# Kernel tuning notes

Hardware: AMD Instinct MI355X
Metric: run time of the kernel (lower is better)

The kernel has to match this reference:

```python
import jax, jax.numpy as jnp
import numpy as np

B, N, D = 8, 1024, 1024
E, H = 16, 4096
CAP_FACTOR = 1.25  # training-mode capacity factor
NUM_CLASSES = 345


def setup_inputs() -> dict:
    key = jax.random.key(0)
    k1, k2, k3, k4 = jax.random.split(key, 4)
    inputs = jax.random.normal(k1, (B, N, D), dtype=jnp.float32)
    current_y = jax.random.randint(k2, (B,), 0, NUM_CLASSES, dtype=jnp.int32)
    std1 = 1.0 / np.sqrt(H)  # init_ uses 1/sqrt(last dim)
    std2 = 1.0 / np.sqrt(D)
    w1 = jax.random.uniform(k3, (E, D, H), dtype=jnp.float32, minval=-std1, maxval=std1)
    w2 = jax.random.uniform(k4, (E, H, D), dtype=jnp.float32, minval=-std2, maxval=std2)
    return {"inputs": inputs, "current_y": current_y, "w1": w1, "w2": w2}


def reference(inputs, current_y, w1, w2):
    b, n, d = inputs.shape
    e = w1.shape[0]
    cap = max(min(n, int(n * CAP_FACTOR / e)), 4)  # MIN_EXPERT_CAPACITY=4
    dt = inputs.dtype

    # class-based gating: every token of sample i goes to expert y_i % e
    idx = jnp.broadcast_to(jnp.remainder(current_y, e)[:, None], (b, n))  # (b,n)
    oh = jax.nn.one_hot(idx, e, dtype=dt)                                 # (b,n,e)
    # exclusive cumsum over token dim, masked
    pos = (jnp.cumsum(oh, axis=-2) - oh) * oh                             # (b,n,e)
    mask1 = oh * (pos < cap).astype(dt)                                   # drop overflow tokens
    mask1_flat = mask1.sum(axis=-1)                                       # (b,n)
    pos_flat = pos.sum(axis=-1).astype(jnp.int32)                         # (b,n)

    # combine[b,n,e,c]; out-of-range positions -> zero row (safe_one_hot semantics)
    combine = (mask1_flat[..., None, None]
               * oh[..., None]
               * jax.nn.one_hot(pos_flat, cap, dtype=dt)[..., None, :])
    dispatch = (combine > 0).astype(dt)

    # dispatch tokens to padded expert slots: (e, b, cap, d)
    expert_in = jnp.einsum('bnd,bnec->ebcd', inputs, dispatch).reshape(e, b * cap, d)
    hidden = jax.nn.gelu(jnp.einsum('end,edh->enh', expert_in, w1), approximate=False)
    expert_out = jnp.einsum('enh,ehd->end', hidden, w2).reshape(e, b, cap, d)

    output = jnp.einsum('ebcd,bnec->bnd', expert_out, combine)
    return output
```

## Files before the change

kernel.cpp:

```cpp
#include <hip/hip_runtime.h>
#include <hip/hip_bf16.h>

#define NB   8
#define NTOK 1024
#define DDIM 1024
#define NEXP 16
#define HDIM 4096
#define CAP  80
#define BK   64

using bf16x8 = __attribute__((ext_vector_type(8))) __bf16;
using bf16x4 = __attribute__((ext_vector_type(4))) __bf16;
using f32x4  = __attribute__((ext_vector_type(4))) float;

__global__ __launch_bounds__(256) void moe_g1(
    const float* __restrict__ X, const int* __restrict__ Y,
    const float* __restrict__ W1, __bf16* __restrict__ Hid)
{
    const int b     = blockIdx.y;
    const int e     = Y[b] & (NEXP - 1);
    const int nbase = blockIdx.x * 64;
    const int tid   = threadIdx.x;
    const int w     = tid >> 6;
    const int l     = tid & 63;
    const int q     = l >> 4;
    const int r     = l & 15;
    const int n     = nbase + w * 16 + r;

    __shared__ __bf16 As[CAP][BK + 8];

    const float* Xb  = X  + (size_t)b * NTOK * DDIM;
    const float* W1e = W1 + (size_t)e * DDIM * HDIM;

    f32x4 acc[5];
    #pragma unroll
    for (int i = 0; i < 5; ++i) acc[i] = f32x4{0.f, 0.f, 0.f, 0.f};

    for (int k0 = 0; k0 < DDIM; k0 += BK) {
        float bv[16];
        const float* bp = W1e + (size_t)(k0 + q * 8) * HDIM + n;
        #pragma unroll
        for (int s = 0; s < 2; ++s)
            #pragma unroll
            for (int j = 0; j < 8; ++j)
                bv[s * 8 + j] = bp[(size_t)(s * 32 + j) * HDIM];

        __syncthreads();
        #pragma unroll
        for (int it = 0; it < 5; ++it) {
            int i   = tid + 256 * it;
            int row = i >> 4, kg = i & 15;
            float4 v = *(const float4*)&Xb[(size_t)row * DDIM + k0 + kg * 4];
            bf16x4 p = {(__bf16)v.x, (__bf16)v.y, (__bf16)v.z, (__bf16)v.w};
            *(bf16x4*)&As[row][kg * 4] = p;
        }
        __syncthreads();

        #pragma unroll
        for (int s = 0; s < 2; ++s) {
            bf16x8 bf;
            #pragma unroll
            for (int j = 0; j < 8; ++j) bf[j] = (__bf16)bv[s * 8 + j];
            #pragma unroll
            for (int mt = 0; mt < 5; ++mt) {
                bf16x8 af = *(const bf16x8*)&As[mt * 16 + r][s * 32 + q * 8];
                acc[mt] = __builtin_amdgcn_mfma_f32_16x16x32_bf16(af, bf, acc[mt], 0, 0, 0);
            }
        }
    }

    __bf16* Hb = Hid + (size_t)b * CAP * HDIM;
    #pragma unroll
    for (int mt = 0; mt < 5; ++mt)
        #pragma unroll
        for (int v = 0; v < 4; ++v) {
            int m = mt * 16 + q * 4 + v;
            float x = acc[mt][v];
            float g = 0.5f * x * (1.0f + erff(x * 0.70710678118654752f));
            Hb[(size_t)m * HDIM + n] = (__bf16)g;
        }
}

__global__ __launch_bounds__(256) void moe_g2(
    const __bf16* __restrict__ Hid, const int* __restrict__ Y,
    const float* __restrict__ W2, float* __restrict__ Out)
{
    const int b     = blockIdx.y;
    const int e     = Y[b] & (NEXP - 1);
    const int nbase = blockIdx.x * 64;
    const int kz    = blockIdx.z * (HDIM / 4);
    const int tid   = threadIdx.x;
    const int w     = tid >> 6;
    const int l     = tid & 63;
    const int q     = l >> 4;
    const int r     = l & 15;
    const int n     = nbase + w * 16 + r;

    __shared__ __bf16 As[CAP][BK + 8];

    const __bf16* Hb  = Hid + (size_t)b * CAP * HDIM;
    const float*  W2e = W2  + (size_t)e * HDIM * DDIM;

    f32x4 acc[5];
    #pragma unroll
    for (int i = 0; i < 5; ++i) acc[i] = f32x4{0.f, 0.f, 0.f, 0.f};

    for (int k0 = kz; k0 < kz + HDIM / 4; k0 += BK) {
        float bv[16];
        const float* bp = W2e + (size_t)(k0 + q * 8) * DDIM + n;
        #pragma unroll
        for (int s = 0; s < 2; ++s)
            #pragma unroll
            for (int j = 0; j < 8; ++j)
                bv[s * 8 + j] = bp[(size_t)(s * 32 + j) * DDIM];

        __syncthreads();
        #pragma unroll
        for (int it = 0; it < 5; ++it) {
            int i   = tid + 256 * it;
            int row = i >> 4, kg = i & 15;
            uint2 v = *(const uint2*)&Hb[(size_t)row * HDIM + k0 + kg * 4];
            *(uint2*)&As[row][kg * 4] = v;
        }
        __syncthreads();

        #pragma unroll
        for (int s = 0; s < 2; ++s) {
            bf16x8 bf;
            #pragma unroll
            for (int j = 0; j < 8; ++j) bf[j] = (__bf16)bv[s * 8 + j];
            #pragma unroll
            for (int mt = 0; mt < 5; ++mt) {
                bf16x8 af = *(const bf16x8*)&As[mt * 16 + r][s * 32 + q * 8];
                acc[mt] = __builtin_amdgcn_mfma_f32_16x16x32_bf16(af, bf, acc[mt], 0, 0, 0);
            }
        }
    }

    float* Ob = Out + (size_t)b * NTOK * DDIM;
    #pragma unroll
    for (int mt = 0; mt < 5; ++mt)
        #pragma unroll
        for (int v = 0; v < 4; ++v) {
            int m = mt * 16 + q * 4 + v;
            atomicAdd(&Ob[(size_t)m * DDIM + n], acc[mt][v]);
        }
}

extern "C" void kernel_launch(void* const* d_in, const int* in_sizes, int n_in,
                              void* d_out, int out_size, void* d_ws, size_t ws_size,
                              hipStream_t stream) {
    const float* X  = (const float*)d_in[0];
    const int*   Y  = (const int*)d_in[1];
    const float* W1 = (const float*)d_in[2];
    const float* W2 = (const float*)d_in[3];
    float*  Out = (float*)d_out;
    __bf16* Hid = (__bf16*)d_ws;

    hipMemsetAsync(d_out, 0, (size_t)out_size * sizeof(float), stream);

    moe_g1<<<dim3(HDIM / 64, NB), 256, 0, stream>>>(X, Y, W1, Hid);
    moe_g2<<<dim3(DDIM / 64, NB, 4), 256, 0, stream>>>(Hid, Y, W2, Out);
}
```

Measured before the change: 475.2 us.

## Double-buffer LDS tiles with register prefetch and transpose weights via LDS

Both GEMM kernels now stage the weight tile through shared memory. Each thread loads it as float4 vectors and transposes it into a bf16 Bt buffer, replacing the per-thread strided scalar loads. Shared A and B tiles are double-buffered, and the next K-slice is prefetched into registers while MFMAs run on the current buffer, which leaves one barrier per iteration. This aims to improve global load coalescing and overlap memory latency with compute, at the cost of more LDS and registers.

```diff
diff --git a/kernel.cpp b/kernel.cpp
--- a/kernel.cpp
+++ b/kernel.cpp
@@ -8,6 +8,7 @@
 #define HDIM 4096
 #define CAP  80
 #define BK   64
+#define LDA  (BK + 8)
 
 using bf16x8 = __attribute__((ext_vector_type(8))) __bf16;
 using bf16x4 = __attribute__((ext_vector_type(4))) __bf16;
@@ -26,8 +27,13 @@
     const int q     = l >> 4;
     const int r     = l & 15;
     const int n     = nbase + w * 16 + r;
-
-    __shared__ __bf16 As[CAP][BK + 8];
+    const int kb    = tid & 15;
+    const int hb    = tid >> 4;
+    const int arow  = tid >> 4;
+    const int akg   = tid & 15;
+
+    __shared__ __bf16 As[2][CAP][LDA];
+    __shared__ __bf16 Bt[2][64][LDA];
 
     const float* Xb  = X  + (size_t)b * NTOK * DDIM;
     const float* W1e = W1 + (size_t)e * DDIM * HDIM;
@@ -36,37 +42,56 @@
     #pragma unroll
     for (int i = 0; i < 5; ++i) acc[i] = f32x4{0.f, 0.f, 0.f, 0.f};
 
-    for (int k0 = 0; k0 < DDIM; k0 += BK) {
-        float bv[16];
-        const float* bp = W1e + (size_t)(k0 + q * 8) * HDIM + n;
-        #pragma unroll
-        for (int s = 0; s < 2; ++s)
-            #pragma unroll
-            for (int j = 0; j < 8; ++j)
-                bv[s * 8 + j] = bp[(size_t)(s * 32 + j) * HDIM];
-
+    float4 a_reg[5];
+    float4 b_reg[4];
+
+    #pragma unroll
+    for (int it = 0; it < 5; ++it)
+        a_reg[it] = *(const float4*)&Xb[(size_t)(arow + 16 * it) * DDIM + akg * 4];
+    #pragma unroll
+    for (int kk = 0; kk < 4; ++kk)
+        b_reg[kk] = *(const float4*)&W1e[(size_t)(kb * 4 + kk) * HDIM + nbase + hb * 4];
+
+    int cur = 0;
+    for (int t = 0; t < DDIM / BK; ++t) {
+        #pragma unroll
+        for (int it = 0; it < 5; ++it) {
+            float4 v = a_reg[it];
+            bf16x4 p = {(__bf16)v.x, (__bf16)v.y, (__bf16)v.z, (__bf16)v.w};
+            *(bf16x4*)&As[cur][arow + 16 * it][akg * 4] = p;
+        }
+        {
+            bf16x4 p0 = {(__bf16)b_reg[0].x, (__bf16)b_reg[1].x, (__bf16)b_reg[2].x, (__bf16)b_reg[3].x};
+            bf16x4 p1 = {(__bf16)b_reg[0].y, (__bf16)b_reg[1].y, (__bf16)b_reg[2].y, (__bf16)b_reg[3].y};
+            bf16x4 p2 = {(__bf16)b_reg[0].z, (__bf16)b_reg[1].z, (__bf16)b_reg[2].z, (__bf16)b_reg[3].z};
+            bf16x4 p3 = {(__bf16)b_reg[0].w, (__bf16)b_reg[1].w, (__bf16)b_reg[2].w, (__bf16)b_reg[3].w};
+            *(bf16x4*)&Bt[cur][hb * 4 + 0][kb * 4] = p0;
+            *(bf16x4*)&Bt[cur][hb * 4 + 1][kb * 4] = p1;
+            *(bf16x4*)&Bt[cur][hb * 4 + 2][kb * 4] = p2;
+            *(bf16x4*)&Bt[cur][hb * 4 + 3][kb * 4] = p3;
+        }
         __syncthreads();
-        #pragma unroll
-        for (int it = 0; it < 5; ++it) {
-            int i   = tid + 256 * it;
-            int row = i >> 4, kg = i & 15;
-            float4 v = *(const float4*)&Xb[(size_t)row * DDIM + k0 + kg * 4];
-            bf16x4 p = {(__bf16)v.x, (__bf16)v.y, (__bf16)v.z, (__bf16)v.w};
-            *(bf16x4*)&As[row][kg * 4] = p;
-        }
-        __syncthreads();
+
+        if (t + 1 < DDIM / BK) {
+            const int k0 = (t + 1) * BK;
+            #pragma unroll
+            for (int it = 0; it < 5; ++it)
+                a_reg[it] = *(const float4*)&Xb[(size_t)(arow + 16 * it) * DDIM + k0 + akg * 4];
+            #pragma unroll
+            for (int kk = 0; kk < 4; ++kk)
+                b_reg[kk] = *(const float4*)&W1e[(size_t)(k0 + kb * 4 + kk) * HDIM + nbase + hb * 4];
+        }
 
         #pragma unroll
         for (int s = 0; s < 2; ++s) {
-            bf16x8 bf;
-            #pragma unroll
-            for (int j = 0; j < 8; ++j) bf[j] = (__bf16)bv[s * 8 + j];
+            bf16x8 bf = *(const bf16x8*)&Bt[cur][w * 16 + r][s * 32 + q * 8];
             #pragma unroll
             for (int mt = 0; mt < 5; ++mt) {
-                bf16x8 af = *(const bf16x8*)&As[mt * 16 + r][s * 32 + q * 8];
+                bf16x8 af = *(const bf16x8*)&As[cur][mt * 16 + r][s * 32 + q * 8];
                 acc[mt] = __builtin_amdgcn_mfma_f32_16x16x32_bf16(af, bf, acc[mt], 0, 0, 0);
             }
         }
+        cur ^= 1;
     }
 
     __bf16* Hb = Hid + (size_t)b * CAP * HDIM;
@@ -95,8 +120,13 @@
     const int q     = l >> 4;
     const int r     = l & 15;
     const int n     = nbase + w * 16 + r;
-
-    __shared__ __bf16 As[CAP][BK + 8];
+    const int kb    = tid & 15;
+    const int hb    = tid >> 4;
+    const int arow  = tid >> 4;
+    const int akg   = tid & 15;
+
+    __shared__ __bf16 As[2][CAP][LDA];
+    __shared__ __bf16 Bt[2][64][LDA];
 
     const __bf16* Hb  = Hid + (size_t)b * CAP * HDIM;
     const float*  W2e = W2  + (size_t)e * HDIM * DDIM;
@@ -105,36 +135,53 @@
     #pragma unroll
     for (int i = 0; i < 5; ++i) acc[i] = f32x4{0.f, 0.f, 0.f, 0.f};
 
-    for (int k0 = kz; k0 < kz + HDIM / 4; k0 += BK) {
-        float bv[16];
-        const float* bp = W2e + (size_t)(k0 + q * 8) * DDIM + n;
-        #pragma unroll
-        for (int s = 0; s < 2; ++s)
-            #pragma unroll
-            for (int j = 0; j < 8; ++j)
-                bv[s * 8 + j] = bp[(size_t)(s * 32 + j) * DDIM];
-
+    uint2  a_reg[5];
+    float4 b_reg[4];
+
+    #pragma unroll
+    for (int it = 0; it < 5; ++it)
+        a_reg[it] = *(const uint2*)&Hb[(size_t)(arow + 16 * it) * HDIM + kz + akg * 4];
+    #pragma unroll
+    for (int kk = 0; kk < 4; ++kk)
+        b_reg[kk] = *(const float4*)&W2e[(size_t)(kz + kb * 4 + kk) * DDIM + nbase + hb * 4];
+
+    int cur = 0;
+    for (int t = 0; t < (HDIM / 4) / BK; ++t) {
+        #pragma unroll
+        for (int it = 0; it < 5; ++it)
+            *(uint2*)&As[cur][arow + 16 * it][akg * 4] = a_reg[it];
+        {
+            bf16x4 p0 = {(__bf16)b_reg[0].x, (__bf16)b_reg[1].x, (__bf16)b_reg[2].x, (__bf16)b_reg[3].x};
+            bf16x4 p1 = {(__bf16)b_reg[0].y, (__bf16)b_reg[1].y, (__bf16)b_reg[2].y, (__bf16)b_reg[3].y};
+            bf16x4 p2 = {(__bf16)b_reg[0].z, (__bf16)b_reg[1].z, (__bf16)b_reg[2].z, (__bf16)b_reg[3].z};
+            bf16x4 p3 = {(__bf16)b_reg[0].w, (__bf16)b_reg[1].w, (__bf16)b_reg[2].w, (__bf16)b_reg[3].w};
+            *(bf16x4*)&Bt[cur][hb * 4 + 0][kb * 4] = p0;
+            *(bf16x4*)&Bt[cur][hb * 4 + 1][kb * 4] = p1;
+            *(bf16x4*)&Bt[cur][hb * 4 + 2][kb * 4] = p2;
+            *(bf16x4*)&Bt[cur][hb * 4 + 3][kb * 4] = p3;
+        }
         __syncthreads();
-        #pragma unroll
-        for (int it = 0; it < 5; ++it) {
-            int i   = tid + 256 * it;
-            int row = i >> 4, kg = i & 15;
-            uint2 v = *(const uint2*)&Hb[(size_t)row * HDIM + k0 + kg * 4];
-            *(uint2*)&As[row][kg * 4] = v;
-        }
-        __syncthreads();
+
+        if (t + 1 < (HDIM / 4) / BK) {
+            const int k0 = kz + (t + 1) * BK;
+            #pragma unroll
+            for (int it = 0; it < 5; ++it)
+                a_reg[it] = *(const uint2*)&Hb[(size_t)(arow + 16 * it) * HDIM + k0 + akg * 4];
+            #pragma unroll
+            for (int kk = 0; kk < 4; ++kk)
+                b_reg[kk] = *(const float4*)&W2e[(size_t)(k0 + kb * 4 + kk) * DDIM + nbase + hb * 4];
+        }
 
         #pragma unroll
         for (int s = 0; s < 2; ++s) {
-            bf16x8 bf;
-            #pragma unroll
-            for (int j = 0; j < 8; ++j) bf[j] = (__bf16)bv[s * 8 + j];
+            bf16x8 bf = *(const bf16x8*)&Bt[cur][w * 16 + r][s * 32 + q * 8];
             #pragma unroll
             for (int mt = 0; mt < 5; ++mt) {
-                bf16x8 af = *(const bf16x8*)&As[mt * 16 + r][s * 32 + q * 8];
+                bf16x8 af = *(const bf16x8*)&As[cur][mt * 16 + r][s * 32 + q * 8];
                 acc[mt] = __builtin_amdgcn_mfma_f32_16x16x32_bf16(af, bf, acc[mt], 0, 0, 0);
             }
         }
+        cur ^= 1;
     }
 
     float* Ob = Out + (size_t)b * NTOK * DDIM;
```

Measured after the change: 484.3 us. No clear change (+1.9%).
